# Performance work log

Hardware: AMD Instinct MI355X
Metric: run time of the kernel (lower is better)

Reference implementation:

```python
import jax, jax.numpy as jnp
import numpy as np

N_EMBD = 1024
N_HEAD = 16
HEAD_DIM = N_EMBD // N_HEAD
D_FF = 4 * N_EMBD
B, T = 2, 2048


def setup_inputs() -> dict:
    key = jax.random.key(0)
    ks = jax.random.split(key, 16)
    s = 0.02
    d = {
        'x': jax.random.normal(ks[0], (B, T, N_EMBD), jnp.float32),
        'ln1_g': jnp.ones((N_EMBD,), jnp.float32),
        'ln1_b': jnp.zeros((N_EMBD,), jnp.float32),
        'Wq': jax.random.normal(ks[1], (N_EMBD, N_EMBD), jnp.float32) * s,
        'bq': jnp.zeros((N_EMBD,), jnp.float32),
        'Wk': jax.random.normal(ks[2], (N_EMBD, N_EMBD), jnp.float32) * s,
        'bk': jnp.zeros((N_EMBD,), jnp.float32),
        'Wv': jax.random.normal(ks[3], (N_EMBD, N_EMBD), jnp.float32) * s,
        'bv': jnp.zeros((N_EMBD,), jnp.float32),
        'Wo': jax.random.normal(ks[4], (N_EMBD, N_EMBD), jnp.float32) * s,
        'bo': jnp.zeros((N_EMBD,), jnp.float32),
        'ln2_g': jnp.ones((N_EMBD,), jnp.float32),
        'ln2_b': jnp.zeros((N_EMBD,), jnp.float32),
        'W1': jax.random.normal(ks[5], (N_EMBD, D_FF), jnp.float32) * s,
        'b1': jnp.zeros((D_FF,), jnp.float32),
        'W2': jax.random.normal(ks[6], (D_FF, N_EMBD), jnp.float32) * s,
        'b2': jnp.zeros((N_EMBD,), jnp.float32),
    }
    return d


def _layernorm(x, g, b, eps=1e-5):
    mu = jnp.mean(x, axis=-1, keepdims=True)
    var = jnp.var(x, axis=-1, keepdims=True)
    return (x - mu) * jax.lax.rsqrt(var + eps) * g + b


def _attention(x, Wq, bq, Wk, bk, Wv, bv, Wo, bo):
    b, t, c = x.shape
    q = (x @ Wq + bq).reshape(b, t, N_HEAD, HEAD_DIM).transpose(0, 2, 1, 3)
    k = (x @ Wk + bk).reshape(b, t, N_HEAD, HEAD_DIM).transpose(0, 2, 1, 3)
    v = (x @ Wv + bv).reshape(b, t, N_HEAD, HEAD_DIM).transpose(0, 2, 1, 3)
    att = jnp.einsum('bhqd,bhkd->bhqk', q, k) / jnp.sqrt(jnp.float32(HEAD_DIM))
    causal = jnp.tril(jnp.ones((t, t), bool))
    att = jnp.where(causal[None, None], att, -jnp.inf)
    att = jax.nn.softmax(att, axis=-1)
    y = jnp.einsum('bhqk,bhkd->bhqd', att, v)
    y = y.transpose(0, 2, 1, 3).reshape(b, t, c)
    return y @ Wo + bo


def reference(x, ln1_g, ln1_b, Wq, bq, Wk, bk, Wv, bv, Wo, bo, ln2_g, ln2_b, W1, b1, W2, b2):
    x = x + _attention(_layernorm(x, ln1_g, ln1_b), Wq, bq, Wk, bk, Wv, bv, Wo, bo)
    h = _layernorm(x, ln2_g, ln2_b)
    h = jax.nn.gelu(h @ W1 + b1, approximate=False) @ W2 + b2
    return x + h
```

## Files before the change

### kernel.cpp

```cpp
#include <hip/hip_runtime.h>
#include <hip/hip_bf16.h>

typedef __hip_bfloat16 bf16;
using bf16x8 = __attribute__((ext_vector_type(8))) short;
using f32x4  = __attribute__((ext_vector_type(4))) float;

#define TSEQ 2048
#define NH   16
#define HD   64
#define NC   1024
#define DFF  4096
#define NROWS 4096

__device__ __forceinline__ void load_lds16(const bf16* g, bf16* l) {
  __builtin_amdgcn_global_load_lds(
      (const __attribute__((address_space(1))) unsigned int*)g,
      (__attribute__((address_space(3))) unsigned int*)l, 16, 0, 0);
}

__device__ __forceinline__ float b2f(short s) {
  unsigned int u = ((unsigned int)(unsigned short)s) << 16;
  return __builtin_bit_cast(float, u);
}

__device__ __forceinline__ float gelu_f(float x) {
  float u = 0.7978845608028654f * fmaf(0.044715f * x, x * x, x);
  float e = __expf(2.0f * u);
  float t = 1.0f - 2.0f / (e + 1.0f);
  return 0.5f * x * (1.0f + t);
}

__global__ __launch_bounds__(256)
void ln_cast_kernel(const float* __restrict__ x, const float* __restrict__ g,
                    const float* __restrict__ b, bf16* __restrict__ out) {
  int row = blockIdx.x, tid = threadIdx.x;
  const float4 v = ((const float4*)(x + (size_t)row * NC))[tid];
  float s  = v.x + v.y + v.z + v.w;
  float s2 = v.x*v.x + v.y*v.y + v.z*v.z + v.w*v.w;
#pragma unroll
  for (int m = 1; m < 64; m <<= 1) { s += __shfl_xor(s, m); s2 += __shfl_xor(s2, m); }
  __shared__ float rs[4], rs2[4];
  if ((tid & 63) == 0) { rs[tid >> 6] = s; rs2[tid >> 6] = s2; }
  __syncthreads();
  s  = rs[0] + rs[1] + rs[2] + rs[3];
  s2 = rs2[0] + rs2[1] + rs2[2] + rs2[3];
  float mu   = s * (1.0f / NC);
  float var  = s2 * (1.0f / NC) - mu * mu;
  float rstd = rsqrtf(var + 1e-5f);
  const float4 gv = ((const float4*)g)[tid];
  const float4 bv = ((const float4*)b)[tid];
  bf16* o = out + (size_t)row * NC + tid * 4;
  o[0] = __float2bfloat16((v.x - mu) * rstd * gv.x + bv.x);
  o[1] = __float2bfloat16((v.y - mu) * rstd * gv.y + bv.y);
  o[2] = __float2bfloat16((v.z - mu) * rstd * gv.z + bv.z);
  o[3] = __float2bfloat16((v.w - mu) * rstd * gv.w + bv.w);
}

__global__ __launch_bounds__(256)
void wo_ln_kernel(const float* __restrict__ x, const float* __restrict__ bo,
                  const bf16* __restrict__ P, const float* __restrict__ g,
                  const float* __restrict__ bln, float* __restrict__ x2,
                  bf16* __restrict__ xn2) {
  int row = blockIdx.x, tid = threadIdx.x;
  size_t base = (size_t)row * NC + tid * 4;
  const float4 xv = *(const float4*)(x + base);
  const float4 bv = ((const float4*)bo)[tid];
  short4 p0 = *(const short4*)((const short*)P + base);
  short4 p1 = *(const short4*)((const short*)P + (size_t)NROWS * NC + base);
  float v0 = xv.x + bv.x + b2f(p0.x) + b2f(p1.x);
  float v1 = xv.y + bv.y + b2f(p0.y) + b2f(p1.y);
  float v2 = xv.z + bv.z + b2f(p0.z) + b2f(p1.z);
  float v3 = xv.w + bv.w + b2f(p0.w) + b2f(p1.w);
  float4 ov = {v0, v1, v2, v3};
  *(float4*)(x2 + base) = ov;
  float s  = v0 + v1 + v2 + v3;
  float s2 = v0*v0 + v1*v1 + v2*v2 + v3*v3;
#pragma unroll
  for (int m = 1; m < 64; m <<= 1) { s += __shfl_xor(s, m); s2 += __shfl_xor(s2, m); }
  __shared__ float rs[4], rs2[4];
  if ((tid & 63) == 0) { rs[tid >> 6] = s; rs2[tid >> 6] = s2; }
  __syncthreads();
  s  = rs[0] + rs[1] + rs[2] + rs[3];
  s2 = rs2[0] + rs2[1] + rs2[2] + rs2[3];
  float mu   = s * (1.0f / NC);
  float var  = s2 * (1.0f / NC) - mu * mu;
  float rstd = rsqrtf(var + 1e-5f);
  const float4 gv = ((const float4*)g)[tid];
  const float4 lv = ((const float4*)bln)[tid];
  bf16* o = xn2 + base;
  o[0] = __float2bfloat16((v0 - mu) * rstd * gv.x + lv.x);
  o[1] = __float2bfloat16((v1 - mu) * rstd * gv.y + lv.y);
  o[2] = __float2bfloat16((v2 - mu) * rstd * gv.z + lv.z);
  o[3] = __float2bfloat16((v3 - mu) * rstd * gv.w + lv.w);
}

__global__ __launch_bounds__(256)
void w2_final_kernel(const float* __restrict__ x2, const float* __restrict__ b2,
                     const bf16* __restrict__ P, float* __restrict__ out) {
  int row = blockIdx.x, tid = threadIdx.x;
  size_t base = (size_t)row * NC + tid * 4;
  const float4 xv = *(const float4*)(x2 + base);
  const float4 bv = ((const float4*)b2)[tid];
  float a0 = xv.x + bv.x, a1 = xv.y + bv.y, a2 = xv.z + bv.z, a3 = xv.w + bv.w;
#pragma unroll
  for (int z = 0; z < 4; ++z) {
    short4 p = *(const short4*)((const short*)P + (size_t)z * NROWS * NC + base);
    a0 += b2f(p.x); a1 += b2f(p.y); a2 += b2f(p.z); a3 += b2f(p.w);
  }
  float4 ov = {a0, a1, a2, a3};
  *(float4*)(out + base) = ov;
}

__global__ __launch_bounds__(256)
void transpose_all_kernel(const float* __restrict__ Wq, const float* __restrict__ Wk,
                          const float* __restrict__ Wv, const float* __restrict__ Wo,
                          const float* __restrict__ W1, const float* __restrict__ W2,
                          bf16* __restrict__ WqkvoT, bf16* __restrict__ W1T,
                          bf16* __restrict__ W2T) {
  int bid = blockIdx.x;
  const float* W; bf16* Wt; int K, N, nx, tile;
  if (bid < 4096) {
    int z = bid >> 10; tile = bid & 1023;
    W = (z == 0) ? Wq : (z == 1) ? Wk : (z == 2) ? Wv : Wo;
    Wt = WqkvoT + (size_t)z * NC * NC; K = NC; N = NC; nx = 32;
  } else if (bid < 8192) {
    tile = bid - 4096; W = W1; Wt = W1T; K = NC; N = DFF; nx = 128;
  } else {
    tile = bid - 8192; W = W2; Wt = W2T; K = DFF; N = NC; nx = 32;
  }
  int n0 = (tile % nx) * 32, k0 = (tile / nx) * 32;
  __shared__ float t[32][33];
  int tx = threadIdx.x, ty = threadIdx.y;
#pragma unroll
  for (int i = 0; i < 4; ++i)
    t[ty + i * 8][tx] = W[(size_t)(k0 + ty + i * 8) * N + n0 + tx];
  __syncthreads();
#pragma unroll
  for (int i = 0; i < 4; ++i)
    Wt[(size_t)(n0 + ty + i * 8) * K + k0 + tx] = __float2bfloat16(t[tx][ty + i * 8]);
}

#define MODE_GELU 4
#define MODE_QKV  5
#define MODE_PART 6

template <int MODE>
__global__ __launch_bounds__(256)
void gemm_bt(const bf16* __restrict__ A, const bf16* __restrict__ Bt,
             const float* __restrict__ bias, const float* __restrict__ bias2,
             const float* __restrict__ bias3,
             void* __restrict__ outp, void* __restrict__ out2, void* __restrict__ out3,
             int M, int N, int K, int KS) {
  __shared__ bf16 As[128 * 32];
  __shared__ bf16 Bs[128 * 32];
  int tid  = threadIdx.x;
  int w    = tid >> 6;
  int lane = tid & 63;
  int l16  = lane & 15;
  int quad = lane >> 4;
  int waveM = (w >> 1) * 64, waveN = (w & 1) * 64;

  int gN = gridDim.x, gM = gridDim.y;
  int pid = blockIdx.y * gN + blockIdx.x;
  int npg = 8 * gN;
  int gid = pid / npg;
  int fm  = gid * 8;
  int gsz = min(gM - fm, 8);
  int bm = (fm + (pid % gsz)) * 128;
  int bn = ((pid % npg) / gsz) * 128;

  int k_beg = blockIdx.z * KS;
  int ldrow = lane >> 2;
  int ldcol = (lane & 3) * 8;

  const bf16* pA[2]; const bf16* pB[2];
#pragma unroll
  for (int i = 0; i < 2; ++i) {
    int r = (w * 2 + i) * 16 + ldrow;
    pA[i] = A  + (size_t)(bm + r) * K + k_beg + ldcol;
    pB[i] = Bt + (size_t)(bn + r) * K + k_beg + ldcol;
  }

  f32x4 acc[4][4];
#pragma unroll
  for (int i = 0; i < 4; ++i)
#pragma unroll
    for (int j = 0; j < 4; ++j) acc[i][j] = (f32x4){0.f, 0.f, 0.f, 0.f};

  for (int k0 = 0; k0 < KS; k0 += 32) {
    __syncthreads();
#pragma unroll
    for (int i = 0; i < 2; ++i) {
      int c = w * 2 + i;
      load_lds16(pA[i], &As[c * 16 * 32]);
      load_lds16(pB[i], &Bs[c * 16 * 32]);
      pA[i] += 32; pB[i] += 32;
    }
    __syncthreads();
    bf16x8 af[4], bfr[4];
#pragma unroll
    for (int mi = 0; mi < 4; ++mi)
      af[mi] = *(const bf16x8*)&As[(waveM + mi * 16 + l16) * 32 + quad * 8];
#pragma unroll
    for (int ni = 0; ni < 4; ++ni)
      bfr[ni] = *(const bf16x8*)&Bs[(waveN + ni * 16 + l16) * 32 + quad * 8];
#pragma unroll
    for (int mi = 0; mi < 4; ++mi)
#pragma unroll
      for (int ni = 0; ni < 4; ++ni)
        acc[mi][ni] = __builtin_amdgcn_mfma_f32_16x16x32_bf16(af[mi], bfr[ni], acc[mi][ni], 0, 0, 0);
  }

  if (MODE == MODE_PART) {
    bf16* dst = (bf16*)outp + (size_t)blockIdx.z * M * N;
#pragma unroll
    for (int mi = 0; mi < 4; ++mi)
#pragma unroll
      for (int r = 0; r < 4; ++r) {
        int row = bm + waveM + mi * 16 + quad * 4 + r;
#pragma unroll
        for (int ni = 0; ni < 4; ++ni) {
          int col = bn + waveN + ni * 16 + l16;
          dst[(size_t)row * N + col] = __float2bfloat16(acc[mi][ni][r]);
        }
      }
  } else if (MODE == MODE_GELU) {
    float bcol[4];
#pragma unroll
    for (int ni = 0; ni < 4; ++ni) bcol[ni] = bias[bn + waveN + ni * 16 + l16];
#pragma unroll
    for (int mi = 0; mi < 4; ++mi)
#pragma unroll
      for (int r = 0; r < 4; ++r) {
        int row = bm + waveM + mi * 16 + quad * 4 + r;
#pragma unroll
        for (int ni = 0; ni < 4; ++ni) {
          int col = bn + waveN + ni * 16 + l16;
          ((bf16*)outp)[(size_t)row * N + col] =
              __float2bfloat16(gelu_f(acc[mi][ni][r] + bcol[ni]));
        }
      }
  } else {
    int seg = bn >> 10;
    int c1b = (bn & (NC - 1)) + waveN;
    const float* bp = (seg == 0) ? bias : (seg == 1) ? bias2 : bias3;
    float bcol[4]; int hh[4], dd[4];
#pragma unroll
    for (int ni = 0; ni < 4; ++ni) {
      int c1 = c1b + ni * 16 + l16;
      bcol[ni] = bp[c1]; hh[ni] = c1 >> 6; dd[ni] = c1 & (HD - 1);
    }
    if (seg < 2) {
      bf16* dst = (seg == 0) ? (bf16*)outp : (bf16*)out2;
#pragma unroll
      for (int mi = 0; mi < 4; ++mi)
#pragma unroll
        for (int r = 0; r < 4; ++r) {
          int row = bm + waveM + mi * 16 + quad * 4 + r;
          int bbi = row >> 11, t = row & (TSEQ - 1);
#pragma unroll
          for (int ni = 0; ni < 4; ++ni)
            dst[((size_t)(bbi * NH + hh[ni]) * TSEQ + t) * HD + dd[ni]] =
                __float2bfloat16(acc[mi][ni][r] + bcol[ni]);
        }
    } else {
      bf16* dst = (bf16*)out3;
#pragma unroll
      for (int mi = 0; mi < 4; ++mi)
#pragma unroll
        for (int r = 0; r < 4; ++r) {
          int row = bm + waveM + mi * 16 + quad * 4 + r;
          int bbi = row >> 11, t = row & (TSEQ - 1);
#pragma unroll
          for (int ni = 0; ni < 4; ++ni)
            dst[((size_t)(bbi * NH + hh[ni]) * HD + dd[ni]) * TSEQ + t] =
                __float2bfloat16(acc[mi][ni][r] + bcol[ni]);
        }
    }
  }
}

__global__ __launch_bounds__(256)
void attn_kernel(const bf16* __restrict__ q, const bf16* __restrict__ k,
                 const bf16* __restrict__ vT, bf16* __restrict__ out) {
  int j = blockIdx.x, h = blockIdx.y, b = blockIdx.z;
  int tid = threadIdx.x, w = tid >> 6, lane = tid & 63;
  int l16 = lane & 15, quad = lane >> 4;
  int tlo = j, thi = 31 - j;
  int qlo0 = tlo * 64 + w * 16;
  int qhi0 = thi * 64 + w * 16;
  const bf16* qp = q  + (size_t)(b * NH + h) * TSEQ * HD;
  const bf16* kp = k  + (size_t)(b * NH + h) * TSEQ * HD;
  const bf16* vp = vT + (size_t)(b * NH + h) * HD * TSEQ;

  __shared__ bf16 Ks[2][64 * 64];
  __shared__ bf16 Vs[2][64 * 64];
  __shared__ bf16 Pw[4][16 * 64];

  bf16x8 qfl[2], qfh[2];
  qfl[0] = *(const bf16x8*)(qp + (size_t)(qlo0 + l16) * HD + quad * 8);
  qfl[1] = *(const bf16x8*)(qp + (size_t)(qlo0 + l16) * HD + 32 + quad * 8);
  qfh[0] = *(const bf16x8*)(qp + (size_t)(qhi0 + l16) * HD + quad * 8);
  qfh[1] = *(const bf16x8*)(qp + (size_t)(qhi0 + l16) * HD + 32 + quad * 8);

  f32x4 ol[4], oh[4];
  float ll[4], lh[4];
#pragma unroll
  for (int i = 0; i < 4; ++i) {
    ol[i] = (f32x4){0.f, 0.f, 0.f, 0.f};
    oh[i] = (f32x4){0.f, 0.f, 0.f, 0.f};
    ll[i] = 0.f; lh[i] = 0.f;
  }

  int lrow = lane >> 3;
  int lc   = (lane & 7) ^ lrow;

  auto stage = [&](int kt, int bi) {
    int kj0 = kt * 64;
#pragma unroll
    for (int i = 0; i < 2; ++i) {
      int c2 = i * 4 + w;
      int row = c2 * 8 + lrow;
      load_lds16(kp + (size_t)(kj0 + row) * HD + lc * 8, &Ks[bi][c2 * 512]);
      load_lds16(vp + (size_t)row * TSEQ + kj0 + lc * 8, &Vs[bi][c2 * 512]);
    }
  };

  auto compute = [&](const bf16x8* qf, int qi0, f32x4* o, float* lacc, int bi, int kj0) {
    float p[4][4];
#pragma unroll
    for (int qq = 0; qq < 4; ++qq) {
      if (kj0 + qq * 16 <= qi0 + 15) {
        f32x4 t = (f32x4){0.f, 0.f, 0.f, 0.f};
        int krow = qq * 16 + l16;
        bf16x8 kf0 = *(const bf16x8*)&Ks[bi][krow * 64 + ((quad       ^ (l16 & 7)) * 8)];
        bf16x8 kf1 = *(const bf16x8*)&Ks[bi][krow * 64 + (((quad + 4) ^ (l16 & 7)) * 8)];
        t = __builtin_amdgcn_mfma_f32_16x16x32_bf16(qf[0], kf0, t, 0, 0, 0);
        t = __builtin_amdgcn_mfma_f32_16x16x32_bf16(qf[1], kf1, t, 0, 0, 0);
        int kj = kj0 + qq * 16 + l16;
#pragma unroll
        for (int r = 0; r < 4; ++r) {
          int qi = qi0 + quad * 4 + r;
          float s = (kj <= qi) ? fmaf(t[r], 0.125f, -8.0f) : -INFINITY;
          p[qq][r] = __expf(s);
          lacc[r] += p[qq][r];
        }
      } else {
#pragma unroll
        for (int r = 0; r < 4; ++r) p[qq][r] = 0.f;
      }
    }
#pragma unroll
    for (int qq = 0; qq < 4; ++qq)
#pragma unroll
      for (int r = 0; r < 4; ++r) {
        int prow = quad * 4 + r;
        int c = qq * 2 + (l16 >> 3);
        Pw[w][prow * 64 + ((c ^ (prow & 7)) * 8) + (l16 & 7)] = __float2bfloat16(p[qq][r]);
      }
#pragma unroll
    for (int tc = 0; tc < 2; ++tc) {
      if (kj0 + tc * 32 <= qi0 + 15) {
        bf16x8 pf = *(const bf16x8*)&Pw[w][l16 * 64 + (((tc * 4 + quad) ^ (l16 & 7)) * 8)];
#pragma unroll
        for (int dn = 0; dn < 4; ++dn) {
          int vrow = dn * 16 + l16;
          bf16x8 vf = *(const bf16x8*)&Vs[bi][vrow * 64 + (((tc * 4 + quad) ^ (l16 & 7)) * 8)];
          o[dn] = __builtin_amdgcn_mfma_f32_16x16x32_bf16(pf, vf, o[dn], 0, 0, 0);
        }
      }
    }
  };

  int nkt = thi + 1;
  stage(0, 0);
  for (int kt = 0; kt < nkt; ++kt) {
    int bi = kt & 1;
    __syncthreads();
    if (kt + 1 < nkt) stage(kt + 1, 1 - bi);
    compute(qfh, qhi0, oh, lh, bi, kt * 64);
    if (kt <= tlo) compute(qfl, qlo0, ol, ll, bi, kt * 64);
  }

#pragma unroll
  for (int m = 1; m < 16; m <<= 1)
#pragma unroll
    for (int r = 0; r < 4; ++r) {
      ll[r] += __shfl_xor(ll[r], m);
      lh[r] += __shfl_xor(lh[r], m);
    }
#pragma unroll
  for (int dn = 0; dn < 4; ++dn)
#pragma unroll
    for (int r = 0; r < 4; ++r) {
      int tl = qlo0 + quad * 4 + r;
      int th = qhi0 + quad * 4 + r;
      out[((size_t)(b * TSEQ + tl)) * NC + h * HD + dn * 16 + l16] = __float2bfloat16(ol[dn][r] / ll[r]);
      out[((size_t)(b * TSEQ + th)) * NC + h * HD + dn * 16 + l16] = __float2bfloat16(oh[dn][r] / lh[r]);
    }
}

extern "C" void kernel_launch(void* const* d_in, const int* in_sizes, int n_in,
                              void* d_out, int out_size, void* d_ws, size_t ws_size,
                              hipStream_t stream) {
  const float* x     = (const float*)d_in[0];
  const float* ln1_g = (const float*)d_in[1];
  const float* ln1_b = (const float*)d_in[2];
  const float* Wq    = (const float*)d_in[3];
  const float* bq    = (const float*)d_in[4];
  const float* Wk    = (const float*)d_in[5];
  const float* bk    = (const float*)d_in[6];
  const float* Wv    = (const float*)d_in[7];
  const float* bv    = (const float*)d_in[8];
  const float* Wo    = (const float*)d_in[9];
  const float* bo    = (const float*)d_in[10];
  const float* ln2_g = (const float*)d_in[11];
  const float* ln2_b = (const float*)d_in[12];
  const float* W1    = (const float*)d_in[13];
  const float* b1    = (const float*)d_in[14];
  const float* W2    = (const float*)d_in[15];
  const float* b2    = (const float*)d_in[16];

  char* ws = (char*)d_ws;
  const size_t MB = 1u << 20;
  bf16* WqkvT = (bf16*)(ws + 0 * MB);
  bf16* W1T  = (bf16*)(ws + 8 * MB);
  bf16* W2T  = (bf16*)(ws + 16 * MB);
  bf16* xn1  = (bf16*)(ws + 24 * MB);
  bf16* qb   = (bf16*)(ws + 32 * MB);
  bf16* kb   = (bf16*)(ws + 40 * MB);
  bf16* vTb  = (bf16*)(ws + 48 * MB);
  bf16* att  = (bf16*)(ws + 56 * MB);
  float* x2  = (float*)(ws + 64 * MB);
  bf16* xn2  = (bf16*)(ws + 80 * MB);
  bf16* h1   = (bf16*)(ws + 88 * MB);
  bf16* woP  = (bf16*)(ws + 88 * MB);
  bf16* w2P  = (bf16*)(ws + 32 * MB);
  bf16* WoT  = WqkvT + 3 * (size_t)NC * NC;

  transpose_all_kernel<<<12288, dim3(32, 8), 0, stream>>>(
      Wq, Wk, Wv, Wo, W1, W2, WqkvT, W1T, W2T);

  ln_cast_kernel<<<NROWS, 256, 0, stream>>>(x, ln1_g, ln1_b, xn1);

  gemm_bt<MODE_QKV><<<dim3(24, 32, 1), 256, 0, stream>>>(
      xn1, WqkvT, bq, bk, bv, qb, kb, vTb, NROWS, 3 * NC, NC, NC);

  attn_kernel<<<dim3(16, NH, 2), 256, 0, stream>>>(qb, kb, vTb, att);

  gemm_bt<MODE_PART><<<dim3(8, 32, 2), 256, 0, stream>>>(
      att, WoT, nullptr, nullptr, nullptr, woP, nullptr, nullptr, NROWS, NC, NC, NC / 2);

  wo_ln_kernel<<<NROWS, 256, 0, stream>>>(x, bo, woP, ln2_g, ln2_b, x2, xn2);

  gemm_bt<MODE_GELU><<<dim3(32, 32, 1), 256, 0, stream>>>(
      xn2, W1T, b1, nullptr, nullptr, h1, nullptr, nullptr, NROWS, DFF, NC, NC);

  gemm_bt<MODE_PART><<<dim3(8, 32, 4), 256, 0, stream>>>(
      h1, W2T, nullptr, nullptr, nullptr, w2P, nullptr, nullptr, NROWS, NC, DFF, DFF / 4);

  w2_final_kernel<<<NROWS, 256, 0, stream>>>(x2, b2, w2P, (float*)d_out);
}
```

Before: 391.1 us.

## Use 32x32x16 MFMA with K=64 tiles and XOR-swizzled LDS in GEMM

The bf16 GEMM now stages K-tiles of 64 instead of 32, halving the number of barrier-separated iterations. It uses 32x32x16 MFMA instructions with a 2x2 accumulator tile per wave in place of 4x4 of 16x16x32. The LDS layout is XOR-swizzled by row so the fragment reads avoid bank conflicts. This doubles LDS use per block and rewrites all epilogue index mappings for the new accumulator layout.

```diff
diff --git a/kernel.cpp b/kernel.cpp
--- a/kernel.cpp
+++ b/kernel.cpp
@@ -4,6 +4,7 @@
 typedef __hip_bfloat16 bf16;
 using bf16x8 = __attribute__((ext_vector_type(8))) short;
 using f32x4  = __attribute__((ext_vector_type(4))) float;
+using f32x16 = __attribute__((ext_vector_type(16))) float;
 
 #define TSEQ 2048
 #define NH   16
@@ -151,13 +152,14 @@
              const float* __restrict__ bias3,
              void* __restrict__ outp, void* __restrict__ out2, void* __restrict__ out3,
              int M, int N, int K, int KS) {
-  __shared__ bf16 As[128 * 32];
-  __shared__ bf16 Bs[128 * 32];
+  __shared__ bf16 As[128 * 64];
+  __shared__ bf16 Bs[128 * 64];
   int tid  = threadIdx.x;
   int w    = tid >> 6;
   int lane = tid & 63;
-  int l16  = lane & 15;
-  int quad = lane >> 4;
+  int l32  = lane & 31;
+  int khalf = lane >> 5;
+  int sx   = lane & 7;
   int waveM = (w >> 1) * 64, waveN = (w & 1) * 64;
 
   int gN = gridDim.x, gM = gridDim.y;
@@ -170,111 +172,116 @@
   int bn = ((pid % npg) / gsz) * 128;
 
   int k_beg = blockIdx.z * KS;
-  int ldrow = lane >> 2;
-  int ldcol = (lane & 3) * 8;
-
-  const bf16* pA[2]; const bf16* pB[2];
-#pragma unroll
-  for (int i = 0; i < 2; ++i) {
-    int r = (w * 2 + i) * 16 + ldrow;
-    pA[i] = A  + (size_t)(bm + r) * K + k_beg + ldcol;
-    pB[i] = Bt + (size_t)(bn + r) * K + k_beg + ldcol;
-  }
-
-  f32x4 acc[4][4];
-#pragma unroll
-  for (int i = 0; i < 4; ++i)
-#pragma unroll
-    for (int j = 0; j < 4; ++j) acc[i][j] = (f32x4){0.f, 0.f, 0.f, 0.f};
-
-  for (int k0 = 0; k0 < KS; k0 += 32) {
+
+  const bf16* pA[4]; const bf16* pB[4];
+#pragma unroll
+  for (int i = 0; i < 4; ++i) {
+    int p = i * 256 + tid;
+    int row = p >> 3;
+    int lc = (p & 7) ^ (row & 7);
+    pA[i] = A  + (size_t)(bm + row) * K + k_beg + lc * 8;
+    pB[i] = Bt + (size_t)(bn + row) * K + k_beg + lc * 8;
+  }
+
+  f32x16 acc[2][2];
+#pragma unroll
+  for (int mi = 0; mi < 2; ++mi)
+#pragma unroll
+    for (int ni = 0; ni < 2; ++ni)
+#pragma unroll
+      for (int r = 0; r < 16; ++r) acc[mi][ni][r] = 0.f;
+
+  for (int kt = 0; kt < KS; kt += 64) {
     __syncthreads();
 #pragma unroll
-    for (int i = 0; i < 2; ++i) {
-      int c = w * 2 + i;
-      load_lds16(pA[i], &As[c * 16 * 32]);
-      load_lds16(pB[i], &Bs[c * 16 * 32]);
-      pA[i] += 32; pB[i] += 32;
+    for (int i = 0; i < 4; ++i) {
+      load_lds16(pA[i], &As[(i * 256 + w * 64) * 8]);
+      load_lds16(pB[i], &Bs[(i * 256 + w * 64) * 8]);
+      pA[i] += 64; pB[i] += 64;
     }
     __syncthreads();
-    bf16x8 af[4], bfr[4];
-#pragma unroll
-    for (int mi = 0; mi < 4; ++mi)
-      af[mi] = *(const bf16x8*)&As[(waveM + mi * 16 + l16) * 32 + quad * 8];
-#pragma unroll
-    for (int ni = 0; ni < 4; ++ni)
-      bfr[ni] = *(const bf16x8*)&Bs[(waveN + ni * 16 + l16) * 32 + quad * 8];
-#pragma unroll
-    for (int mi = 0; mi < 4; ++mi)
-#pragma unroll
-      for (int ni = 0; ni < 4; ++ni)
-        acc[mi][ni] = __builtin_amdgcn_mfma_f32_16x16x32_bf16(af[mi], bfr[ni], acc[mi][ni], 0, 0, 0);
+#pragma unroll
+    for (int s = 0; s < 4; ++s) {
+      int ch = ((s * 2 + khalf) ^ sx) * 8;
+      bf16x8 af[2], bfr[2];
+#pragma unroll
+      for (int mi = 0; mi < 2; ++mi)
+        af[mi] = *(const bf16x8*)&As[(waveM + mi * 32 + l32) * 64 + ch];
+#pragma unroll
+      for (int ni = 0; ni < 2; ++ni)
+        bfr[ni] = *(const bf16x8*)&Bs[(waveN + ni * 32 + l32) * 64 + ch];
+#pragma unroll
+      for (int mi = 0; mi < 2; ++mi)
+#pragma unroll
+        for (int ni = 0; ni < 2; ++ni)
+          acc[mi][ni] = __builtin_amdgcn_mfma_f32_32x32x16_bf16(af[mi], bfr[ni], acc[mi][ni], 0, 0, 0);
+    }
   }
 
   if (MODE == MODE_PART) {
     bf16* dst = (bf16*)outp + (size_t)blockIdx.z * M * N;
 #pragma unroll
-    for (int mi = 0; mi < 4; ++mi)
-#pragma unroll
-      for (int r = 0; r < 4; ++r) {
-        int row = bm + waveM + mi * 16 + quad * 4 + r;
-#pragma unroll
-        for (int ni = 0; ni < 4; ++ni) {
-          int col = bn + waveN + ni * 16 + l16;
-          dst[(size_t)row * N + col] = __float2bfloat16(acc[mi][ni][r]);
+    for (int mi = 0; mi < 2; ++mi)
+#pragma unroll
+      for (int ni = 0; ni < 2; ++ni) {
+        int col = bn + waveN + ni * 32 + l32;
+#pragma unroll
+        for (int reg = 0; reg < 16; ++reg) {
+          int row = bm + waveM + mi * 32 + (reg & 3) + 8 * (reg >> 2) + 4 * khalf;
+          dst[(size_t)row * N + col] = __float2bfloat16(acc[mi][ni][reg]);
         }
       }
   } else if (MODE == MODE_GELU) {
-    float bcol[4];
-#pragma unroll
-    for (int ni = 0; ni < 4; ++ni) bcol[ni] = bias[bn + waveN + ni * 16 + l16];
-#pragma unroll
-    for (int mi = 0; mi < 4; ++mi)
-#pragma unroll
-      for (int r = 0; r < 4; ++r) {
-        int row = bm + waveM + mi * 16 + quad * 4 + r;
-#pragma unroll
-        for (int ni = 0; ni < 4; ++ni) {
-          int col = bn + waveN + ni * 16 + l16;
+    float bcol[2];
+#pragma unroll
+    for (int ni = 0; ni < 2; ++ni) bcol[ni] = bias[bn + waveN + ni * 32 + l32];
+#pragma unroll
+    for (int mi = 0; mi < 2; ++mi)
+#pragma unroll
+      for (int ni = 0; ni < 2; ++ni) {
+        int col = bn + waveN + ni * 32 + l32;
+#pragma unroll
+        for (int reg = 0; reg < 16; ++reg) {
+          int row = bm + waveM + mi * 32 + (reg & 3) + 8 * (reg >> 2) + 4 * khalf;
           ((bf16*)outp)[(size_t)row * N + col] =
-              __float2bfloat16(gelu_f(acc[mi][ni][r] + bcol[ni]));
+              __float2bfloat16(gelu_f(acc[mi][ni][reg] + bcol[ni]));
         }
       }
   } else {
     int seg = bn >> 10;
     int c1b = (bn & (NC - 1)) + waveN;
     const float* bp = (seg == 0) ? bias : (seg == 1) ? bias2 : bias3;
-    float bcol[4]; int hh[4], dd[4];
-#pragma unroll
-    for (int ni = 0; ni < 4; ++ni) {
-      int c1 = c1b + ni * 16 + l16;
+    float bcol[2]; int hh[2], dd[2];
+#pragma unroll
+    for (int ni = 0; ni < 2; ++ni) {
+      int c1 = c1b + ni * 32 + l32;
       bcol[ni] = bp[c1]; hh[ni] = c1 >> 6; dd[ni] = c1 & (HD - 1);
     }
     if (seg < 2) {
       bf16* dst = (seg == 0) ? (bf16*)outp : (bf16*)out2;
 #pragma unroll
-      for (int mi = 0; mi < 4; ++mi)
-#pragma unroll
-        for (int r = 0; r < 4; ++r) {
-          int row = bm + waveM + mi * 16 + quad * 4 + r;
+      for (int mi = 0; mi < 2; ++mi)
+#pragma unroll
+        for (int reg = 0; reg < 16; ++reg) {
+          int row = bm + waveM + mi * 32 + (reg & 3) + 8 * (reg >> 2) + 4 * khalf;
           int bbi = row >> 11, t = row & (TSEQ - 1);
 #pragma unroll
-          for (int ni = 0; ni < 4; ++ni)
+          for (int ni = 0; ni < 2; ++ni)
             dst[((size_t)(bbi * NH + hh[ni]) * TSEQ + t) * HD + dd[ni]] =
-                __float2bfloat16(acc[mi][ni][r] + bcol[ni]);
+                __float2bfloat16(acc[mi][ni][reg] + bcol[ni]);
         }
     } else {
       bf16* dst = (bf16*)out3;
 #pragma unroll
-      for (int mi = 0; mi < 4; ++mi)
-#pragma unroll
-        for (int r = 0; r < 4; ++r) {
-          int row = bm + waveM + mi * 16 + quad * 4 + r;
+      for (int mi = 0; mi < 2; ++mi)
+#pragma unroll
+        for (int reg = 0; reg < 16; ++reg) {
+          int row = bm + waveM + mi * 32 + (reg & 3) + 8 * (reg >> 2) + 4 * khalf;
           int bbi = row >> 11, t = row & (TSEQ - 1);
 #pragma unroll
-          for (int ni = 0; ni < 4; ++ni)
+          for (int ni = 0; ni < 2; ++ni)
             dst[((size_t)(bbi * NH + hh[ni]) * HD + dd[ni]) * TSEQ + t] =
-                __float2bfloat16(acc[mi][ni][r] + bcol[ni]);
+                __float2bfloat16(acc[mi][ni][reg] + bcol[ni]);
         }
     }
   }
```

Result: faster. 366.5 us (-6.3%).
